# Performance work log

Hardware: AMD Instinct MI355X
Metric: run time of the kernel (lower is better)

Reference implementation:

```python
import jax, jax.numpy as jnp
import numpy as np

L, B, T, C, H, DF, V = 6, 8, 1024, 768, 12, 3072, 512
HD = C // H  # head_dim = 64
STD = 0.02
EPS = 1e-5


def layernorm(x, g, b):
    mu = jnp.mean(x, axis=-1, keepdims=True)
    var = jnp.mean(jnp.square(x - mu), axis=-1, keepdims=True)
    return (x - mu) * jax.lax.rsqrt(var + EPS) * g + b


def setup_inputs() -> dict:
    key = jax.random.key(0)
    ks = jax.random.split(key, 8)
    # weights stored as [in, out] so forward is x @ W (== torch x @ W.T)
    tok_emb = jax.random.normal(ks[0], (V, C), jnp.float32) * STD
    pos_emb = jax.random.normal(ks[1], (T, C), jnp.float32) * STD
    Wqkv = jax.random.normal(ks[2], (L, C, 3 * C), jnp.float32) * STD
    Wproj = jax.random.normal(ks[3], (L, C, C), jnp.float32) * STD
    W1 = jax.random.normal(ks[4], (L, C, DF), jnp.float32) * STD
    b1 = jnp.zeros((L, DF), jnp.float32)
    W2 = jax.random.normal(ks[5], (L, DF, C), jnp.float32) * STD
    b2 = jnp.zeros((L, C), jnp.float32)
    ln1_g = jnp.ones((L, C), jnp.float32); ln1_b = jnp.zeros((L, C), jnp.float32)
    ln2_g = jnp.ones((L, C), jnp.float32); ln2_b = jnp.zeros((L, C), jnp.float32)
    lnf_g = jnp.ones((C,), jnp.float32); lnf_b = jnp.zeros((C,), jnp.float32)
    idx = jax.random.randint(ks[6], (B, T), 0, V, jnp.int64 if jax.config.jax_enable_x64 else jnp.int32)
    return {"idx": idx, "tok_emb": tok_emb, "pos_emb": pos_emb, "Wqkv": Wqkv,
            "Wproj": Wproj, "W1": W1, "b1": b1, "W2": W2, "b2": b2,
            "ln1_g": ln1_g, "ln1_b": ln1_b, "ln2_g": ln2_g, "ln2_b": ln2_b,
            "lnf_g": lnf_g, "lnf_b": lnf_b}


def reference(idx, tok_emb, pos_emb, Wqkv, Wproj, W1, b1, W2, b2,
              ln1_g, ln1_b, ln2_g, ln2_b, lnf_g, lnf_b):
    Bx, Tx = idx.shape
    x = tok_emb[idx] + pos_emb[:Tx][None, :, :]  # [B,T,C]
    causal = jnp.triu(jnp.ones((Tx, Tx), bool), k=1)  # True above diagonal
    scale = np.sqrt(HD).astype(np.float32)
    neg_inf = jnp.asarray(-jnp.inf, x.dtype)
    for l in range(L):
        # --- causal self-attention ---
        xn = layernorm(x, ln1_g[l], ln1_b[l])
        qkv = jnp.einsum('btc,cd->btd', xn, Wqkv[l])  # [B,T,3C]
        q, k, v = jnp.split(qkv, 3, axis=-1)
        q = q.reshape(Bx, Tx, H, HD)
        k = k.reshape(Bx, Tx, H, HD)
        v = v.reshape(Bx, Tx, H, HD)
        scores = jnp.einsum('bthd,bshd->bhts', q, k) / scale  # [B,H,T,T]
        scores = jnp.where(causal, neg_inf, scores)
        w = jax.nn.softmax(scores, axis=-1)
        attn = jnp.einsum('bhts,bshd->bthd', w, v).reshape(Bx, Tx, C)
        x = x + jnp.einsum('btc,cd->btd', attn, Wproj[l])
        # --- MLP ---
        xn = layernorm(x, ln2_g[l], ln2_b[l])
        h = jax.nn.gelu(jnp.einsum('btc,cf->btf', xn, W1[l]) + b1[l], approximate=False)
        x = x + jnp.einsum('btf,fc->btc', h, W2[l]) + b2[l]
    logits = jnp.einsum('btc,vc->btv', layernorm(x, lnf_g, lnf_b), tok_emb)  # tied head
    return logits
```

## Files before the change

### kernel.cpp

```cpp
#include <hip/hip_runtime.h>
#include <hip/hip_bf16.h>
#include <stdint.h>

#define LNUM 6
#define BB 8
#define TT 1024
#define CC 768
#define HH 12
#define HDIM 64
#define DFF 3072
#define VV 512
#define MM (BB*TT)
#define QKREG ((size_t)BB*HH*TT*64)

typedef __bf16 bf16x8 __attribute__((ext_vector_type(8)));
typedef float f32x4 __attribute__((ext_vector_type(4)));

__device__ __forceinline__ uint16_t f2b(float f) {
  uint32_t u = __float_as_uint(f);
  u += 0x7FFFu + ((u >> 16) & 1u);
  return (uint16_t)(u >> 16);
}

__device__ __forceinline__ float b2f(uint16_t u) {
  return __uint_as_float((uint32_t)u << 16);
}

__device__ __forceinline__ void gld16(const uint16_t* g, uint16_t* l) {
  __builtin_amdgcn_global_load_lds(
      (const __attribute__((address_space(1))) uint32_t*)g,
      (__attribute__((address_space(3))) uint32_t*)l, 16, 0, 0);
}

__device__ __forceinline__ f32x4 mfma16(bf16x8 a, bf16x8 b, f32x4 c) {
  return __builtin_amdgcn_mfma_f32_16x16x32_bf16(a, b, c, 0, 0, 0);
}

__global__ __launch_bounds__(256) void cvt4_k(const float* __restrict__ in,
                                              uint16_t* __restrict__ out, int n4) {
  const int gid = blockIdx.x * 256 + threadIdx.x;
  if (gid >= n4) return;
  const float4 v = ((const float4*)in)[gid];
  ushort4 w; w.x = f2b(v.x); w.y = f2b(v.y); w.z = f2b(v.z); w.w = f2b(v.w);
  ((ushort4*)out)[gid] = w;
}

__global__ __launch_bounds__(256) void embed_k(const int* __restrict__ idx,
                                               const float* __restrict__ tok,
                                               const float* __restrict__ pos,
                                               uint16_t* __restrict__ x) {
  const int gid = blockIdx.x * 256 + threadIdx.x;
  const int row = gid / (CC / 4), c4 = gid % (CC / 4);
  const int t = row & (TT - 1);
  const int tkn = idx[row];
  const float4 a = ((const float4*)(tok + (size_t)tkn * CC))[c4];
  const float4 q = ((const float4*)(pos + (size_t)t * CC))[c4];
  ushort4 w;
  w.x = f2b(a.x + q.x); w.y = f2b(a.y + q.y);
  w.z = f2b(a.z + q.z); w.w = f2b(a.w + q.w);
  ((ushort4*)(x + (size_t)row * CC))[c4] = w;
}

__global__ __launch_bounds__(256) void ln_k(const uint16_t* __restrict__ x,
                                            const float* __restrict__ gamma,
                                            const float* __restrict__ beta,
                                            uint16_t* __restrict__ o) {
  const int lane = threadIdx.x & 63, wid = threadIdx.x >> 6;
  const int row = blockIdx.x * 4 + wid;
  const ushort4* xr = (const ushort4*)(x + (size_t)row * CC);
  float4 v[3]; float s = 0.f, sq = 0.f;
#pragma unroll
  for (int i = 0; i < 3; ++i) {
    const ushort4 u = xr[lane + i * 64];
    v[i] = make_float4(b2f(u.x), b2f(u.y), b2f(u.z), b2f(u.w));
    s += v[i].x + v[i].y + v[i].z + v[i].w;
    sq += v[i].x * v[i].x + v[i].y * v[i].y + v[i].z * v[i].z + v[i].w * v[i].w;
  }
#pragma unroll
  for (int m = 1; m < 64; m <<= 1) { s += __shfl_xor(s, m, 64); sq += __shfl_xor(sq, m, 64); }
  const float mu = s * (1.f / 768.f);
  const float rstd = rsqrtf(sq * (1.f / 768.f) - mu * mu + 1e-5f);
  ushort4* orow = (ushort4*)(o + (size_t)row * CC);
#pragma unroll
  for (int i = 0; i < 3; ++i) {
    const int c4 = lane + i * 64;
    const float4 gg = ((const float4*)gamma)[c4];
    const float4 bb = ((const float4*)beta)[c4];
    ushort4 w;
    w.x = f2b((v[i].x - mu) * rstd * gg.x + bb.x);
    w.y = f2b((v[i].y - mu) * rstd * gg.y + bb.y);
    w.z = f2b((v[i].z - mu) * rstd * gg.z + bb.z);
    w.w = f2b((v[i].w - mu) * rstd * gg.w + bb.w);
    orow[c4] = w;
  }
}

template <int NP>
__global__ __launch_bounds__(256) void lnrb_k(uint16_t* __restrict__ x,
                                              const uint16_t* __restrict__ pp,
                                              const float* __restrict__ gamma,
                                              const float* __restrict__ beta,
                                              uint16_t* __restrict__ o) {
  const int lane = threadIdx.x & 63, wid = threadIdx.x >> 6;
  const int row = blockIdx.x * 4 + wid;
  ushort4* xr = (ushort4*)(x + (size_t)row * CC);
  float4 v[3]; float s = 0.f, sq = 0.f;
#pragma unroll
  for (int i = 0; i < 3; ++i) {
    const int c4 = lane + i * 64;
    const ushort4 u = xr[c4];
    float4 a = make_float4(b2f(u.x), b2f(u.y), b2f(u.z), b2f(u.w));
#pragma unroll
    for (int j = 0; j < NP; ++j) {
      const ushort4 q =
          ((const ushort4*)(pp + (size_t)j * MM * CC + (size_t)row * CC))[c4];
      a.x += b2f(q.x); a.y += b2f(q.y); a.z += b2f(q.z); a.w += b2f(q.w);
    }
    ushort4 w;
    w.x = f2b(a.x); w.y = f2b(a.y); w.z = f2b(a.z); w.w = f2b(a.w);
    xr[c4] = w;
    v[i] = a;
    s += a.x + a.y + a.z + a.w;
    sq += a.x * a.x + a.y * a.y + a.z * a.z + a.w * a.w;
  }
#pragma unroll
  for (int m = 1; m < 64; m <<= 1) { s += __shfl_xor(s, m, 64); sq += __shfl_xor(sq, m, 64); }
  const float mu = s * (1.f / 768.f);
  const float rstd = rsqrtf(sq * (1.f / 768.f) - mu * mu + 1e-5f);
  ushort4* orow = (ushort4*)(o + (size_t)row * CC);
#pragma unroll
  for (int i = 0; i < 3; ++i) {
    const int c4 = lane + i * 64;
    const float4 gg = ((const float4*)gamma)[c4];
    const float4 bb = ((const float4*)beta)[c4];
    ushort4 w;
    w.x = f2b((v[i].x - mu) * rstd * gg.x + bb.x);
    w.y = f2b((v[i].y - mu) * rstd * gg.y + bb.y);
    w.z = f2b((v[i].z - mu) * rstd * gg.z + bb.z);
    w.w = f2b((v[i].w - mu) * rstd * gg.w + bb.w);
    orow[c4] = w;
  }
}

__global__ __launch_bounds__(256) void tca_k(const float* __restrict__ Wq,
                                             const float* __restrict__ Wp,
                                             const float* __restrict__ W1p,
                                             const float* __restrict__ W2p,
                                             uint16_t* __restrict__ dq,
                                             uint16_t* __restrict__ dp,
                                             uint16_t* __restrict__ d1,
                                             uint16_t* __restrict__ d2) {
  __shared__ float tile[32][33];
  const int b = blockIdx.x;
  const int l = b / 6912;
  int r = b - l * 6912;
  const float* src; uint16_t* dst; int K, N, kt, nt;
  if (r < 1728) {
    K = CC; N = 3 * CC;
    src = Wq + (size_t)l * CC * 3 * CC; dst = dq + (size_t)l * CC * 3 * CC;
    kt = r / 72; nt = r % 72;
  } else if (r < 2304) {
    r -= 1728; K = CC; N = CC;
    src = Wp + (size_t)l * CC * CC; dst = dp + (size_t)l * CC * CC;
    kt = r / 24; nt = r % 24;
  } else if (r < 4608) {
    r -= 2304; K = CC; N = DFF;
    src = W1p + (size_t)l * CC * DFF; dst = d1 + (size_t)l * CC * DFF;
    kt = r / 96; nt = r % 96;
  } else {
    r -= 4608; K = DFF; N = CC;
    src = W2p + (size_t)l * DFF * CC; dst = d2 + (size_t)l * DFF * CC;
    kt = r / 24; nt = r % 24;
  }
  const int tx = threadIdx.x & 31, ty = threadIdx.x >> 5;
  const int kb = kt * 32, nb = nt * 32;
#pragma unroll
  for (int i = 0; i < 32; i += 8)
    tile[ty + i][tx] = src[(size_t)(kb + ty + i) * N + nb + tx];
  __syncthreads();
#pragma unroll
  for (int i = 0; i < 32; i += 8)
    dst[(size_t)(nb + ty + i) * K + kb + tx] = f2b(tile[tx][ty + i]);
}

template <int EPI>
__global__ __launch_bounds__(256) void gemm_k(const uint16_t* __restrict__ A,
                                              const uint16_t* __restrict__ Bt,
                                              int N, int K,
                                              const float* __restrict__ bias,
                                              uint16_t* __restrict__ outb,
                                              float* __restrict__ outf) {
  __shared__ __align__(16) uint16_t As[128 * 64];
  __shared__ __align__(16) uint16_t Bs[128 * 64];
  const int tid = threadIdx.x;
  const int lane = tid & 63, wid = tid >> 6;
  const int wm = wid >> 1, wn = wid & 1;
  const int bm = blockIdx.x * 128, bn = blockIdx.y * 128;
  const int kp = blockIdx.z;
  const int Ksub = K / (int)gridDim.z;
  const int k0b = kp * Ksub;
  const int nkt = Ksub >> 6;
  const int srow = tid >> 3;
  const int swz = (tid & 7) ^ (srow & 7);
  const uint16_t* gA0 = A + (size_t)(bm + srow) * K + k0b + swz * 8;
  const uint16_t* gB0 = Bt + (size_t)(bn + srow) * K + k0b + swz * 8;
  const size_t qs = (size_t)32 * K;
  const int l15 = lane & 15, lhi = lane >> 4;
  int aof[2][4], bof[2][4];
#pragma unroll
  for (int kk = 0; kk < 2; ++kk)
#pragma unroll
    for (int i = 0; i < 4; ++i) {
      const int sw = ((kk * 4 + lhi) ^ (l15 & 7)) * 16;
      aof[kk][i] = (wm * 64 + i * 16 + l15) * 128 + sw;
      bof[kk][i] = (wn * 64 + i * 16 + l15) * 128 + sw;
    }
  f32x4 acc[4][4] = {};
  for (int t = 0; t < nkt; ++t) {
    const int ko = t * 64;
#pragma unroll
    for (int q = 0; q < 4; ++q) {
      gld16(gA0 + q * qs + ko, &As[q * 2048 + tid * 8]);
      gld16(gB0 + q * qs + ko, &Bs[q * 2048 + tid * 8]);
    }
    __syncthreads();
    const char* Ab = (const char*)As;
    const char* Bb = (const char*)Bs;
#pragma unroll
    for (int kk = 0; kk < 2; ++kk) {
      bf16x8 a[4], b[4];
#pragma unroll
      for (int i = 0; i < 4; ++i) {
        a[i] = *(const bf16x8*)(Ab + aof[kk][i]);
        b[i] = *(const bf16x8*)(Bb + bof[kk][i]);
      }
#pragma unroll
      for (int i = 0; i < 4; ++i)
#pragma unroll
        for (int j = 0; j < 4; ++j)
          acc[i][j] = mfma16(a[i], b[j], acc[i][j]);
    }
    __syncthreads();
  }
#pragma unroll
  for (int i = 0; i < 4; ++i) {
    const int m0 = bm + wm * 64 + i * 16 + (lhi << 2);
#pragma unroll
    for (int j = 0; j < 4; ++j) {
      const int n = bn + wn * 64 + j * 16 + l15;
      if constexpr (EPI == 5) {
        const int sec = n / CC;
        const int rn = n - sec * CC;
        const int hh = rn >> 6, d = rn & 63;
        const int b = m0 >> 10, t0 = m0 & 1023;
        if (sec == 2) {
          ushort4 w;
          w.x = f2b(acc[i][j][0]); w.y = f2b(acc[i][j][1]);
          w.z = f2b(acc[i][j][2]); w.w = f2b(acc[i][j][3]);
          *(ushort4*)(outb + 2 * QKREG + ((size_t)(b * HH + hh) * 64 + d) * TT + t0) = w;
        } else {
          uint16_t* dst = outb + (size_t)sec * QKREG + ((size_t)(b * HH + hh) * TT + t0) * 64 + d;
#pragma unroll
          for (int rr = 0; rr < 4; ++rr) dst[(size_t)rr * 64] = f2b(acc[i][j][rr]);
        }
      } else if constexpr (EPI == 8) {
        uint16_t* pdst = outb + (size_t)kp * ((size_t)MM * N);
        const float bb = (kp == 0 && bias) ? bias[n] : 0.f;
#pragma unroll
        for (int rr = 0; rr < 4; ++rr)
          pdst[(size_t)(m0 + rr) * N + n] = f2b(acc[i][j][rr] + bb);
      } else {
#pragma unroll
        for (int rr = 0; rr < 4; ++rr) {
          const size_t o = (size_t)(m0 + rr) * N + n;
          const float v = acc[i][j][rr];
          if constexpr (EPI == 1) {
            outf[o] = v;
          } else if constexpr (EPI == 2) {
            float t = v + bias[n];
            t = 0.5f * t * (1.0f + erff(t * 0.70710678118654752f));
            outb[o] = f2b(t);
          }
        }
      }
    }
  }
}

__global__ __launch_bounds__(256) void attn_k(const uint16_t* __restrict__ qkvh,
                                              uint16_t* __restrict__ ao) {
  __shared__ __align__(16) uint16_t Ks[2][64 * 64], Vs[2][64 * 64];
  __shared__ __align__(16) uint16_t Ps[4][16 * 64];
  const int tid = threadIdx.x, lane = tid & 63, wid = tid >> 6;
  const int qt = (TT / 64 - 1) - blockIdx.x / (BB * HH);
  const int bh = blockIdx.x % (BB * HH);
  const uint16_t* qb = qkvh + (size_t)bh * (TT * 64);
  const uint16_t* kb = qkvh + QKREG + (size_t)bh * (TT * 64);
  const uint16_t* vb = qkvh + 2 * QKREG + (size_t)bh * ((size_t)64 * TT);
  const int l15 = lane & 15, lhi = lane >> 4;
  bf16x8 qf[2];
  {
    const uint16_t* qr = qb + (size_t)(qt * 64 + wid * 16 + l15) * 64 + lhi * 8;
    qf[0] = *(const bf16x8*)qr;
    qf[1] = *(const bf16x8*)(qr + 32);
  }
  const int c0 = tid, c1 = tid + 256;
  const int r0 = c0 >> 3, r1 = c1 >> 3;
  const int cb0 = (c0 & 7) * 16, cb1 = (c1 & 7) * 16;
  const int ph0 = r0 * 128 + (cb0 ^ ((r0 & 7) << 4));
  const int ph1 = r1 * 128 + (cb1 ^ ((r1 & 7) << 4));

  uint4 kr0, kr1, vr0, vr1;
  kr0 = *(const uint4*)(kb + (size_t)r0 * 64 + cb0 / 2);
  kr1 = *(const uint4*)(kb + (size_t)r1 * 64 + cb1 / 2);
  vr0 = *(const uint4*)(vb + (size_t)r0 * TT + cb0 / 2);
  vr1 = *(const uint4*)(vb + (size_t)r1 * TT + cb1 / 2);
  *(uint4*)((char*)Ks[0] + ph0) = kr0;
  *(uint4*)((char*)Ks[0] + ph1) = kr1;
  *(uint4*)((char*)Vs[0] + ph0) = vr0;
  *(uint4*)((char*)Vs[0] + ph1) = vr1;

  f32x4 oacc[4] = {};
  float mrun[4] = {-INFINITY, -INFINITY, -INFINITY, -INFINITY};
  float lrun[4] = {0.f, 0.f, 0.f, 0.f};
  char* pb = (char*)Ps[wid];

  for (int j = 0; j <= qt; ++j) {
    const int cur = j & 1;
    const bool more = (j < qt);
    __syncthreads();
    if (more) {
      const int jn = (j + 1) * 64;
      kr0 = *(const uint4*)(kb + (size_t)(jn + r0) * 64 + cb0 / 2);
      kr1 = *(const uint4*)(kb + (size_t)(jn + r1) * 64 + cb1 / 2);
      vr0 = *(const uint4*)(vb + (size_t)r0 * TT + jn + cb0 / 2);
      vr1 = *(const uint4*)(vb + (size_t)r1 * TT + jn + cb1 / 2);
    }
    const char* Kb = (const char*)Ks[cur];
    const char* Vb = (const char*)Vs[cur];
    f32x4 s4[4] = {};
    __builtin_amdgcn_s_setprio(1);
#pragma unroll
    for (int kk = 0; kk < 2; ++kk) {
      const int cbyte = kk * 64 + lhi * 16;
#pragma unroll
      for (int nt = 0; nt < 4; ++nt) {
        const int krow = nt * 16 + l15;
        const bf16x8 kf = *(const bf16x8*)(Kb + krow * 128 + (cbyte ^ ((krow & 7) << 4)));
        s4[nt] = mfma16(qf[kk], kf, s4[nt]);
      }
    }
    __builtin_amdgcn_s_setprio(0);
    const bool diag = (j == qt);
    float alpha[4];
#pragma unroll
    for (int r = 0; r < 4; ++r) {
      const int qg = qt * 64 + wid * 16 + (lhi << 2) + r;
      float mx = -INFINITY;
#pragma unroll
      for (int nt = 0; nt < 4; ++nt) {
        float v = s4[nt][r] * 0.125f;
        if (diag && (j * 64 + nt * 16 + l15) > qg) v = -INFINITY;
        s4[nt][r] = v;
        mx = fmaxf(mx, v);
      }
#pragma unroll
      for (int m = 1; m < 16; m <<= 1) mx = fmaxf(mx, __shfl_xor(mx, m, 16));
      const float mnew = fmaxf(mrun[r], mx);
      alpha[r] = __expf(mrun[r] - mnew);
      float ps = 0.f;
#pragma unroll
      for (int nt = 0; nt < 4; ++nt) {
        const float pp = __expf(s4[nt][r] - mnew);
        s4[nt][r] = pp;
        ps += pp;
      }
#pragma unroll
      for (int m = 1; m < 16; m <<= 1) ps += __shfl_xor(ps, m, 16);
      lrun[r] = lrun[r] * alpha[r] + ps;
      mrun[r] = mnew;
    }
#pragma unroll
    for (int dt = 0; dt < 4; ++dt)
#pragma unroll
      for (int r = 0; r < 4; ++r) oacc[dt][r] *= alpha[r];
#pragma unroll
    for (int r = 0; r < 4; ++r) {
      const int prow = (lhi << 2) + r;
      const int swp = (prow & 7) << 4;
#pragma unroll
      for (int nt = 0; nt < 4; ++nt) {
        const int cb = (nt * 16 + l15) * 2;
        *(uint16_t*)(pb + prow * 128 + (cb ^ swp)) = f2b(s4[nt][r]);
      }
    }
    __builtin_amdgcn_s_setprio(1);
#pragma unroll
    for (int kk = 0; kk < 2; ++kk) {
      const int cbyte = kk * 64 + lhi * 16;
      const bf16x8 pf = *(const bf16x8*)(pb + l15 * 128 + (cbyte ^ ((l15 & 7) << 4)));
#pragma unroll
      for (int dt = 0; dt < 4; ++dt) {
        const int vrow = dt * 16 + l15;
        const bf16x8 vf = *(const bf16x8*)(Vb + vrow * 128 + (cbyte ^ ((vrow & 7) << 4)));
        oacc[dt] = mfma16(pf, vf, oacc[dt]);
      }
    }
    __builtin_amdgcn_s_setprio(0);
    if (more) {
      char* kn = (char*)Ks[cur ^ 1];
      char* vn = (char*)Vs[cur ^ 1];
      *(uint4*)(kn + ph0) = kr0;
      *(uint4*)(kn + ph1) = kr1;
      *(uint4*)(vn + ph0) = vr0;
      *(uint4*)(vn + ph1) = vr1;
    }
  }
#pragma unroll
  for (int dt = 0; dt < 4; ++dt) {
#pragma unroll
    for (int r = 0; r < 4; ++r) {
      const int q = qt * 64 + wid * 16 + (lhi << 2) + r;
      const float v = oacc[dt][r] / lrun[r];
      ao[(size_t)((bh / HH) * TT + q) * CC + (bh % HH) * HDIM + dt * 16 + l15] = f2b(v);
    }
  }
}

extern "C" void kernel_launch(void* const* d_in, const int* in_sizes, int n_in,
                              void* d_out, int out_size, void* d_ws, size_t ws_size,
                              hipStream_t stream) {
  (void)in_sizes; (void)n_in; (void)out_size;
  const int*   idx  = (const int*)d_in[0];
  const float* tok  = (const float*)d_in[1];
  const float* pos  = (const float*)d_in[2];
  const float* Wqkv = (const float*)d_in[3];
  const float* Wpro = (const float*)d_in[4];
  const float* W1   = (const float*)d_in[5];
  const float* b1   = (const float*)d_in[6];
  const float* W2   = (const float*)d_in[7];
  const float* b2   = (const float*)d_in[8];
  const float* g1   = (const float*)d_in[9];
  const float* be1  = (const float*)d_in[10];
  const float* g2   = (const float*)d_in[11];
  const float* be2  = (const float*)d_in[12];
  const float* gf   = (const float*)d_in[13];
  const float* bfb  = (const float*)d_in[14];
  float* out = (float*)d_out;

  const size_t QS = (size_t)CC * 3 * CC;
  const size_t PS = (size_t)CC * CC;
  const size_t S1 = (size_t)CC * DFF;
  const size_t S2 = (size_t)DFF * CC;

  char* p = (char*)d_ws;
  uint16_t* x = (uint16_t*)p;      p += (size_t)MM * CC * 2;
  uint16_t* act = (uint16_t*)p;    p += (size_t)MM * CC * 2;
  uint16_t* big = (uint16_t*)p;    p += (size_t)MM * DFF * 2;
  uint16_t* tokb = (uint16_t*)p;   p += (size_t)VV * CC * 2;
  uint16_t* partb = (uint16_t*)p;  p += (size_t)2 * MM * CC * 2;
  char* pbase = p;
  uint16_t* wqA = (uint16_t*)p;    p += QS * LNUM * 2;
  uint16_t* wpA = (uint16_t*)p;    p += PS * LNUM * 2;
  uint16_t* w1A = (uint16_t*)p;    p += S1 * LNUM * 2;
  uint16_t* w2A = (uint16_t*)p;    p += S2 * LNUM * 2;
  const bool roomy2 = ws_size >= (size_t)(p - (char*)d_ws);
  if (!roomy2) {
    p = pbase;
    wqA = (uint16_t*)p; p += QS * 2;
    wpA = (uint16_t*)p; p += PS * 2;
    w1A = (uint16_t*)p; p += S1 * 2;
    w2A = (uint16_t*)p; p += S2 * 2;
  }

  cvt4_k<<<dim3((VV * CC / 4 + 255) / 256), 256, 0, stream>>>(tok, tokb, VV * CC / 4);
  embed_k<<<dim3(MM * (CC / 4) / 256), 256, 0, stream>>>(idx, tok, pos, x);
  ln_k<<<dim3(MM / 4), 256, 0, stream>>>(x, g1, be1, act);
  if (roomy2)
    tca_k<<<dim3(LNUM * 6912), 256, 0, stream>>>(Wqkv, Wpro, W1, W2, wqA, wpA, w1A, w2A);

  for (int l = 0; l < LNUM; ++l) {
    if (!roomy2)
      tca_k<<<dim3(6912), 256, 0, stream>>>(Wqkv + (size_t)l * QS, Wpro + (size_t)l * PS,
                                            W1 + (size_t)l * S1, W2 + (size_t)l * S2,
                                            wqA, wpA, w1A, w2A);
    const size_t lw = roomy2 ? (size_t)l : 0;
    gemm_k<5><<<dim3(MM / 128, 3 * CC / 128, 1), 256, 0, stream>>>(
        act, wqA + lw * QS, 3 * CC, CC, nullptr, big, nullptr);
    attn_k<<<dim3((TT / 64) * BB * HH), 256, 0, stream>>>(big, act);
    gemm_k<8><<<dim3(MM / 128, CC / 128, 2), 256, 0, stream>>>(
        act, wpA + lw * PS, CC, CC, nullptr, partb, nullptr);
    lnrb_k<2><<<dim3(MM / 4), 256, 0, stream>>>(x, partb,
                                                g2 + (size_t)l * CC, be2 + (size_t)l * CC, act);
    gemm_k<2><<<dim3(MM / 128, DFF / 128, 1), 256, 0, stream>>>(
        act, w1A + lw * S1, DFF, CC, b1 + (size_t)l * DFF, big, nullptr);
    const float* ng = (l + 1 < LNUM) ? g1 + (size_t)(l + 1) * CC : gf;
    const float* nb = (l + 1 < LNUM) ? be1 + (size_t)(l + 1) * CC : bfb;
    gemm_k<8><<<dim3(MM / 128, CC / 128, 2), 256, 0, stream>>>(
        big, w2A + lw * S2, CC, DFF, b2 + (size_t)l * CC, partb, nullptr);
    lnrb_k<2><<<dim3(MM / 4), 256, 0, stream>>>(x, partb, ng, nb, act);
  }
  gemm_k<1><<<dim3(MM / 128, VV / 128, 1), 256, 0, stream>>>(
      act, tokb, VV, CC, nullptr, nullptr, out);
}
```

Before: 1.463 ms.

## Widen attention blocks to 128 queries with 8 waves and pack transpose stores

The attention kernel now runs 512 threads per block, covering 128 query rows, so each staged K/V tile is shared by twice as many waves and total K/V reloads from global memory drop. The diagonal mask check becomes per-wave, so waves whose rows lie below a key tile skip masking while the extra causal tile adds some idle work for the lower waves. The weight transpose-convert kernel now handles 64x32 tiles and writes two bf16 values per 32-bit store, halving its block count. The larger attention blocks halve the grid and may reduce occupancy.

```diff
diff --git a/kernel.cpp b/kernel.cpp
--- a/kernel.cpp
+++ b/kernel.cpp
@@ -150,37 +150,41 @@
                                              uint16_t* __restrict__ dp,
                                              uint16_t* __restrict__ d1,
                                              uint16_t* __restrict__ d2) {
-  __shared__ float tile[32][33];
+  __shared__ float tile[64][33];
   const int b = blockIdx.x;
-  const int l = b / 6912;
-  int r = b - l * 6912;
+  const int l = b / 3456;
+  int r = b - l * 3456;
   const float* src; uint16_t* dst; int K, N, kt, nt;
-  if (r < 1728) {
+  if (r < 864) {
     K = CC; N = 3 * CC;
     src = Wq + (size_t)l * CC * 3 * CC; dst = dq + (size_t)l * CC * 3 * CC;
     kt = r / 72; nt = r % 72;
-  } else if (r < 2304) {
-    r -= 1728; K = CC; N = CC;
+  } else if (r < 1152) {
+    r -= 864; K = CC; N = CC;
     src = Wp + (size_t)l * CC * CC; dst = dp + (size_t)l * CC * CC;
     kt = r / 24; nt = r % 24;
-  } else if (r < 4608) {
-    r -= 2304; K = CC; N = DFF;
+  } else if (r < 2304) {
+    r -= 1152; K = CC; N = DFF;
     src = W1p + (size_t)l * CC * DFF; dst = d1 + (size_t)l * CC * DFF;
     kt = r / 96; nt = r % 96;
   } else {
-    r -= 4608; K = DFF; N = CC;
+    r -= 2304; K = DFF; N = CC;
     src = W2p + (size_t)l * DFF * CC; dst = d2 + (size_t)l * DFF * CC;
     kt = r / 24; nt = r % 24;
   }
+  const int kb = kt * 64, nb = nt * 32;
   const int tx = threadIdx.x & 31, ty = threadIdx.x >> 5;
-  const int kb = kt * 32, nb = nt * 32;
-#pragma unroll
-  for (int i = 0; i < 32; i += 8)
+#pragma unroll
+  for (int i = 0; i < 64; i += 8)
     tile[ty + i][tx] = src[(size_t)(kb + ty + i) * N + nb + tx];
   __syncthreads();
 #pragma unroll
-  for (int i = 0; i < 32; i += 8)
-    dst[(size_t)(nb + ty + i) * K + kb + tx] = f2b(tile[tx][ty + i]);
+  for (int i = 0; i < 32; i += 8) {
+    const int n = ty + i;
+    const int k2 = tx * 2;
+    const uint32_t w = (uint32_t)f2b(tile[k2][n]) | ((uint32_t)f2b(tile[k2 + 1][n]) << 16);
+    *(uint32_t*)(dst + (size_t)(nb + n) * K + kb + k2) = w;
+  }
 }
 
 template <int EPI>
@@ -287,12 +291,12 @@
   }
 }
 
-__global__ __launch_bounds__(256) void attn_k(const uint16_t* __restrict__ qkvh,
+__global__ __launch_bounds__(512) void attn_k(const uint16_t* __restrict__ qkvh,
                                               uint16_t* __restrict__ ao) {
   __shared__ __align__(16) uint16_t Ks[2][64 * 64], Vs[2][64 * 64];
-  __shared__ __align__(16) uint16_t Ps[4][16 * 64];
+  __shared__ __align__(16) uint16_t Ps[8][16 * 64];
   const int tid = threadIdx.x, lane = tid & 63, wid = tid >> 6;
-  const int qt = (TT / 64 - 1) - blockIdx.x / (BB * HH);
+  const int p = (TT / 128 - 1) - blockIdx.x / (BB * HH);
   const int bh = blockIdx.x % (BB * HH);
   const uint16_t* qb = qkvh + (size_t)bh * (TT * 64);
   const uint16_t* kb = qkvh + QKREG + (size_t)bh * (TT * 64);
@@ -300,41 +304,35 @@
   const int l15 = lane & 15, lhi = lane >> 4;
   bf16x8 qf[2];
   {
-    const uint16_t* qr = qb + (size_t)(qt * 64 + wid * 16 + l15) * 64 + lhi * 8;
+    const uint16_t* qr = qb + (size_t)(p * 128 + wid * 16 + l15) * 64 + lhi * 8;
     qf[0] = *(const bf16x8*)qr;
     qf[1] = *(const bf16x8*)(qr + 32);
   }
-  const int c0 = tid, c1 = tid + 256;
-  const int r0 = c0 >> 3, r1 = c1 >> 3;
-  const int cb0 = (c0 & 7) * 16, cb1 = (c1 & 7) * 16;
+  const int r0 = tid >> 3;
+  const int cb0 = (tid & 7) * 16;
   const int ph0 = r0 * 128 + (cb0 ^ ((r0 & 7) << 4));
-  const int ph1 = r1 * 128 + (cb1 ^ ((r1 & 7) << 4));
-
-  uint4 kr0, kr1, vr0, vr1;
+
+  uint4 kr0, vr0;
   kr0 = *(const uint4*)(kb + (size_t)r0 * 64 + cb0 / 2);
-  kr1 = *(const uint4*)(kb + (size_t)r1 * 64 + cb1 / 2);
   vr0 = *(const uint4*)(vb + (size_t)r0 * TT + cb0 / 2);
-  vr1 = *(const uint4*)(vb + (size_t)r1 * TT + cb1 / 2);
   *(uint4*)((char*)Ks[0] + ph0) = kr0;
-  *(uint4*)((char*)Ks[0] + ph1) = kr1;
   *(uint4*)((char*)Vs[0] + ph0) = vr0;
-  *(uint4*)((char*)Vs[0] + ph1) = vr1;
 
   f32x4 oacc[4] = {};
   float mrun[4] = {-INFINITY, -INFINITY, -INFINITY, -INFINITY};
   float lrun[4] = {0.f, 0.f, 0.f, 0.f};
   char* pb = (char*)Ps[wid];
-
-  for (int j = 0; j <= qt; ++j) {
+  const int jmax = 2 * p + 1;
+  const int qgmin = p * 128 + wid * 16;
+
+  for (int j = 0; j <= jmax; ++j) {
     const int cur = j & 1;
-    const bool more = (j < qt);
+    const bool more = (j < jmax);
     __syncthreads();
     if (more) {
       const int jn = (j + 1) * 64;
       kr0 = *(const uint4*)(kb + (size_t)(jn + r0) * 64 + cb0 / 2);
-      kr1 = *(const uint4*)(kb + (size_t)(jn + r1) * 64 + cb1 / 2);
       vr0 = *(const uint4*)(vb + (size_t)r0 * TT + jn + cb0 / 2);
-      vr1 = *(const uint4*)(vb + (size_t)r1 * TT + jn + cb1 / 2);
     }
     const char* Kb = (const char*)Ks[cur];
     const char* Vb = (const char*)Vs[cur];
@@ -351,11 +349,11 @@
       }
     }
     __builtin_amdgcn_s_setprio(0);
-    const bool diag = (j == qt);
+    const bool diag = (j * 64 + 63) > qgmin;
     float alpha[4];
 #pragma unroll
     for (int r = 0; r < 4; ++r) {
-      const int qg = qt * 64 + wid * 16 + (lhi << 2) + r;
+      const int qg = qgmin + (lhi << 2) + r;
       float mx = -INFINITY;
 #pragma unroll
       for (int nt = 0; nt < 4; ++nt) {
@@ -411,16 +409,14 @@
       char* kn = (char*)Ks[cur ^ 1];
       char* vn = (char*)Vs[cur ^ 1];
       *(uint4*)(kn + ph0) = kr0;
-      *(uint4*)(kn + ph1) = kr1;
       *(uint4*)(vn + ph0) = vr0;
-      *(uint4*)(vn + ph1) = vr1;
     }
   }
 #pragma unroll
   for (int dt = 0; dt < 4; ++dt) {
 #pragma unroll
     for (int r = 0; r < 4; ++r) {
-      const int q = qt * 64 + wid * 16 + (lhi << 2) + r;
+      const int q = p * 128 + wid * 16 + (lhi << 2) + r;
       const float v = oacc[dt][r] / lrun[r];
       ao[(size_t)((bh / HH) * TT + q) * CC + (bh % HH) * HDIM + dt * 16 + l15] = f2b(v);
     }
@@ -477,17 +473,17 @@
   embed_k<<<dim3(MM * (CC / 4) / 256), 256, 0, stream>>>(idx, tok, pos, x);
   ln_k<<<dim3(MM / 4), 256, 0, stream>>>(x, g1, be1, act);
   if (roomy2)
-    tca_k<<<dim3(LNUM * 6912), 256, 0, stream>>>(Wqkv, Wpro, W1, W2, wqA, wpA, w1A, w2A);
+    tca_k<<<dim3(LNUM * 3456), 256, 0, stream>>>(Wqkv, Wpro, W1, W2, wqA, wpA, w1A, w2A);
 
   for (int l = 0; l < LNUM; ++l) {
     if (!roomy2)
-      tca_k<<<dim3(6912), 256, 0, stream>>>(Wqkv + (size_t)l * QS, Wpro + (size_t)l * PS,
+      tca_k<<<dim3(3456), 256, 0, stream>>>(Wqkv + (size_t)l * QS, Wpro + (size_t)l * PS,
                                             W1 + (size_t)l * S1, W2 + (size_t)l * S2,
                                             wqA, wpA, w1A, w2A);
     const size_t lw = roomy2 ? (size_t)l : 0;
     gemm_k<5><<<dim3(MM / 128, 3 * CC / 128, 1), 256, 0, stream>>>(
         act, wqA + lw * QS, 3 * CC, CC, nullptr, big, nullptr);
-    attn_k<<<dim3((TT / 64) * BB * HH), 256, 0, stream>>>(big, act);
+    attn_k<<<dim3((TT / 128) * BB * HH), 512, 0, stream>>>(big, act);
     gemm_k<8><<<dim3(MM / 128, CC / 128, 2), 256, 0, stream>>>(
         act, wpA + lw * PS, CC, CC, nullptr, partb, nullptr);
     lnrb_k<2><<<dim3(MM / 4), 256, 0, stream>>>(x, partb,
```

After: 1.484 ms (median of 2 runs). Within noise of the previous version (+1.4%).
